# Kernel tuning notes

Hardware: AMD Instinct MI355X
Metric: run time of the kernel (lower is better)

Reference implementation:

```python
import jax, jax.numpy as jnp
import numpy as np

B, N, K = 8, 4096, 5


def setup_inputs() -> dict:
    key = jax.random.key(0)
    ks = jax.random.split(key, 24)
    s = 0.05
    inp = {
        'pointcloud': jax.random.normal(ks[0], (B, 3, N, 1), jnp.float32),
        # local 1x1 conv stack (bias-free) + BN affine params (eval mode, stats=identity)
        'conv_w1': jax.random.normal(ks[1], (64, 3), jnp.float32) * s,
        'bn1_g': jnp.ones((64,), jnp.float32), 'bn1_b': jnp.zeros((64,), jnp.float32),
        'conv_w2': jax.random.normal(ks[2], (64, 64), jnp.float32) * s,
        'bn2_g': jnp.ones((64,), jnp.float32), 'bn2_b': jnp.zeros((64,), jnp.float32),
        'conv_w3': jax.random.normal(ks[3], (64, 64), jnp.float32) * s,
        'bn3_g': jnp.ones((64,), jnp.float32), 'bn3_b': jnp.zeros((64,), jnp.float32),
        'conv_w4': jax.random.normal(ks[4], (128, 64), jnp.float32) * s,
        'bn4_g': jnp.ones((128,), jnp.float32), 'bn4_b': jnp.zeros((128,), jnp.float32),
        # GCN layers
        'gc1_w': jax.random.normal(ks[5], (128, 128), jnp.float32) * s,
        'gc1_b': jnp.zeros((128,), jnp.float32),
        'gc2_w': jax.random.normal(ks[6], (128, 128), jnp.float32) * s,
        'gc2_b': jnp.zeros((128,), jnp.float32),
        'gc3_w': jax.random.normal(ks[7], (128, 256), jnp.float32) * s,
        'gc3_b': jnp.zeros((256,), jnp.float32),
        # MLP head
        'fc1_w': jax.random.normal(ks[8], (512, 256), jnp.float32) * s,
        'bnf1_g': jnp.ones((512,), jnp.float32), 'bnf1_b': jnp.zeros((512,), jnp.float32),
        'fc2_w': jax.random.normal(ks[9], (256, 512), jnp.float32) * s,
        'bnf2_g': jnp.ones((256,), jnp.float32), 'bnf2_b': jnp.zeros((256,), jnp.float32),
        'fc3_w': jax.random.normal(ks[10], (128, 256), jnp.float32) * s,
        'fc3_b': jnp.zeros((128,), jnp.float32),
    }
    return inp


def _cbr(h, w, g, b):
    # 1x1 conv (per-point linear) + BatchNorm(eval, identity stats) + ReLU
    return jax.nn.relu((h @ w.T) * g + b)


def reference(pointcloud, conv_w1, bn1_g, bn1_b, conv_w2, bn2_g, bn2_b,
              conv_w3, bn3_g, bn3_b, conv_w4, bn4_g, bn4_b,
              gc1_w, gc1_b, gc2_w, gc2_b, gc3_w, gc3_b,
              fc1_w, bnf1_g, bnf1_b, fc2_w, bnf2_g, bnf2_b, fc3_w, fc3_b):
    pts = pointcloud[..., 0]                       # [B,3,N]
    b, _, n = pts.shape

    # ---- LocalOperation: sort points by distance to centroid, gather ----
    centroid = pts.mean(axis=2, keepdims=True)     # [B,3,1]
    d_cent = ((pts - centroid) ** 2).sum(axis=1)   # [B,N]
    order = jnp.argsort(d_cent, axis=-1)           # [B,N]
    x = jnp.take_along_axis(pts, order[:, None, :], axis=2)  # [B,3,N]

    h = x.transpose(0, 2, 1)                       # [B,N,3]
    h = _cbr(h, conv_w1, bn1_g, bn1_b)             # [B,N,64]
    h = _cbr(h, conv_w2, bn2_g, bn2_b)
    h = _cbr(h, conv_w3, bn3_g, bn3_b)
    h = _cbr(h, conv_w4, bn4_g, bn4_b)             # [B,N,128]
    feat = h.reshape(b * n, 128)                   # node features

    # ---- KNN graph (k=5, within each cloud, self included like KDTree) ----
    sq = (pts ** 2).sum(axis=1)                                        # [B,N]
    d2 = sq[:, :, None] + sq[:, None, :] - 2.0 * jnp.einsum('bcn,bcm->bnm', pts, pts)
    _, nbr = jax.lax.top_k(-d2, K)                                     # [B,N,K]
    offsets = (jnp.arange(b) * n)[:, None, None]
    src = (nbr + offsets).reshape(-1)                                  # [B*N*K]
    dst = jnp.broadcast_to(jnp.arange(b * n).reshape(b, n, 1), (b, n, K)).reshape(-1)

    num_nodes = b * n
    ones = jnp.ones_like(src, jnp.float32)
    deg_out = jax.ops.segment_sum(ones, src, num_segments=num_nodes)
    deg_in = jax.ops.segment_sum(ones, dst, num_segments=num_nodes)
    norm_out = jax.lax.rsqrt(jnp.maximum(deg_out, 1.0))
    norm_in = jax.lax.rsqrt(jnp.maximum(deg_in, 1.0))

    def gcn(hh, w, bias):
        hw = (hh @ w) * norm_out[:, None]          # [BN,F] pre-normed features
        msg = hw[src]                              # gather
        agg = jax.ops.segment_sum(msg, dst, num_segments=num_nodes)  # scatter-add
        return agg * norm_in[:, None] + bias

    g = jax.nn.relu(gcn(feat, gc1_w, gc1_b))       # [BN,128]
    g = jax.nn.relu(gcn(g, gc2_w, gc2_b))          # [BN,128]
    g = gcn(g, gc3_w, gc3_b)                       # [BN,256]

    # ---- head (BN eval, dropout eval = identity) ----
    z = jax.nn.relu((g @ fc1_w.T) * bnf1_g + bnf1_b)   # [BN,512]
    z = jax.nn.relu((z @ fc2_w.T) * bnf2_g + bnf2_b)   # [BN,256]
    pooled = z.max(axis=0)                             # [256] global max over nodes
    out = pooled @ fc3_w.T + fc3_b                     # [128]
    return out
```

## Files before the change

### kernel.cpp

```cpp
#include <hip/hip_runtime.h>
#include <math.h>
#include <float.h>

#define NB 8
#define NP 4096
#define BN_ (NB*NP)
#define KNN 5
#define JCH 512
#define NJC (NP/JCH)
#define SENT 64

typedef unsigned short u16;
typedef __attribute__((ext_vector_type(8))) __bf16 bf16x8;
typedef __attribute__((ext_vector_type(4))) float f32x4;

__device__ __forceinline__ u16 f2bf(float x){
  unsigned u = __float_as_uint(x);
  u += 0x7fff + ((u>>16)&1);
  return (u16)(u>>16);
}
__device__ __forceinline__ float bf2f(u16 h){ return __uint_as_float(((unsigned)h)<<16); }


__global__ void k_centroid(const float* __restrict__ pc, float* __restrict__ dcent,
                           int* __restrict__ rankb) {
  int b = blockIdx.x, tid = threadIdx.x;
  const float* px = pc + (size_t)b*3*NP;
  const float* py = px + NP;
  const float* pz = py + NP;
  double sx=0, sy=0, sz=0;
  for (int n = tid; n < NP; n += 256) { sx += px[n]; sy += py[n]; sz += pz[n]; }
  __shared__ double rx[256], ry[256], rz[256];
  rx[tid]=sx; ry[tid]=sy; rz[tid]=sz;
  __syncthreads();
  for (int s = 128; s > 0; s >>= 1) {
    if (tid < s) { rx[tid]+=rx[tid+s]; ry[tid]+=ry[tid+s]; rz[tid]+=rz[tid+s]; }
    __syncthreads();
  }
  __shared__ float cxs, cys, czs;
  if (tid == 0) {
    cxs = (float)(rx[0]/NP); cys = (float)(ry[0]/NP); czs = (float)(rz[0]/NP);
  }
  __syncthreads();
  float cx = cxs, cy = cys, cz = czs;
  for (int n = tid; n < NP; n += 256) {
    float dx = __fsub_rn(px[n], cx);
    float dy = __fsub_rn(py[n], cy);
    float dz = __fsub_rn(pz[n], cz);
    float d = __fadd_rn(__fadd_rn(__fmul_rn(dx,dx), __fmul_rn(dy,dy)), __fmul_rn(dz,dz));
    dcent[b*NP + n] = d;
    rankb[b*NP + n] = 0;
  }
}

__global__ void __launch_bounds__(256) k_rank_part(const float* __restrict__ dcent,
                                                   int* __restrict__ rank) {
  int jc = blockIdx.x, ic = blockIdx.y, b = blockIdx.z;
  __shared__ float d[JCH];
  int j0 = jc*JCH;
  for (int n = threadIdx.x; n < JCH; n += 256) d[n] = dcent[b*NP + j0 + n];
  __syncthreads();
  int i = ic*256 + threadIdx.x;
  float di = dcent[b*NP + i];
  int cnt = 0;
  #pragma unroll 8
  for (int n = 0; n < JCH; ++n) {
    float dj = d[n];
    cnt += (dj < di) || (dj == di && (j0 + n) < i);
  }
  atomicAdd(&rank[b*NP + i], cnt);
}

__global__ void k_scatprep(const float* __restrict__ pc, const int* __restrict__ rank,
                           const float* __restrict__ dcent,
                           int* __restrict__ ord, float4* __restrict__ srt,
                           float* __restrict__ rcv, int* __restrict__ deg) {
  int idx = blockIdx.x*256 + threadIdx.x;
  int b = idx >> 12, i = idx & (NP-1);
  int r = rank[idx];
  ord[b*NP + r] = i;
  const float* base = pc + (size_t)b*3*NP;
  float x = base[i], y = base[NP+i], z = base[2*NP+i];
  float sq = __fadd_rn(__fadd_rn(__fmul_rn(x,x), __fmul_rn(y,y)), __fmul_rn(z,z));
  float4 v; v.x=x; v.y=y; v.z=z; v.w=sq;
  srt[b*NP + r] = v;
  rcv[b*NP + r] = sqrtf(dcent[idx]);
  deg[idx] = 0;
}

#define INS(dist, q) \
  if (dist < b4) { \
    if (dist < b3) { b4=b3; r4=r3; \
      if (dist < b2) { b3=b2; r3=r2; \
        if (dist < b1) { b2=b1; r2=r1; \
          if (dist < b0) { b1=b0; r1=r0; b0=dist; r0=(q); } \
          else { b1=dist; r1=(q); } \
        } else { b2=dist; r2=(q); } \
      } else { b3=dist; r3=(q); } \
    } else { b4=dist; r4=(q); } \
  }

__global__ void __launch_bounds__(512) k_knn_ann4(const float4* __restrict__ srt,
                                                  const float* __restrict__ rc,
                                                  const int* __restrict__ ord,
                                                  int* __restrict__ nbr,
                                                  int* __restrict__ deg) {
  __shared__ float4 tile[NP + 2*SENT];
  __shared__ float rtile[NP + 2*SENT];
  int b = blockIdx.x >> 6;
  int blk = blockIdx.x & 63;
  int gbase = b*NP;
  for (int t = threadIdx.x; t < NP + 2*SENT; t += 512) {
    int q = t - SENT;
    if ((unsigned)q < NP) { tile[t] = srt[gbase + q]; rtile[t] = rc[gbase + q]; }
    else { float4 s4; s4.x=0.f; s4.y=0.f; s4.z=0.f; s4.w=1e30f; tile[t] = s4; rtile[t] = 0.f; }
  }
  __syncthreads();

  const int lane = threadIdx.x & 63;
  const int wv   = threadIdx.x >> 6;
  const int grp  = lane >> 3;
  const int sub  = lane & 7;
  const int s_i  = blk*64 + wv*8 + grp;

  float4 p = tile[SENT + s_i];
  float xi=p.x, yi=p.y, zi=p.z, sqi=p.w;
  float ri = rtile[SENT + s_i];

  const bool is_hi = (sub < 4);
  const int step = is_hi ? 4 : -4;
  const int jdead = is_hi ? (NP + 7) : (-36);
  int j = is_hi ? (s_i + sub) : (s_i - 1 - (sub - 4));
  bool alive = ((unsigned)j < NP);
  if (!alive) j = jdead;

  float b0=FLT_MAX, b1=FLT_MAX, b2=FLT_MAX, b3=FLT_MAX, b4=FLT_MAX;
  int r0=0, r1=0, r2=0, r3=0, r4=0;

  while (__ballot(alive)) {
    float4 jp[8];
    #pragma unroll
    for (int t = 0; t < 8; ++t) jp[t] = tile[SENT + j + step*t];
    #pragma unroll
    for (int t = 0; t < 8; ++t) {
      float dot = __fadd_rn(__fadd_rn(__fmul_rn(xi,jp[t].x), __fmul_rn(yi,jp[t].y)), __fmul_rn(zi,jp[t].z));
      float dist = __fsub_rn(__fadd_rn(sqi, jp[t].w), __fmul_rn(2.0f, dot));
      if (__ballot(dist < b4)) { INS(dist, j + step*t) }
    }
    float bm = b4;
    bm = fminf(bm, __shfl_xor(bm, 1));
    bm = fminf(bm, __shfl_xor(bm, 2));
    bm = fminf(bm, __shfl_xor(bm, 4));
    float T = bm*1.0002f + 1e-9f;
    float dr = fabsf(ri - rtile[SENT + j + step*7]);
    bool nextin = ((unsigned)(j + step*8) < NP);
    alive = alive && nextin && (__fmul_rn(dr,dr) < T);
    j = alive ? (j + step*8) : jdead;
  }

  #pragma unroll
  for (int m = 1; m <= 4; m <<= 1) {
    float c0=__shfl_xor(b0,m), c1=__shfl_xor(b1,m), c2=__shfl_xor(b2,m),
          c3=__shfl_xor(b3,m), c4=__shfl_xor(b4,m);
    int   s0=__shfl_xor(r0,m), s1=__shfl_xor(r1,m), s2=__shfl_xor(r2,m),
          s3=__shfl_xor(r3,m), s4=__shfl_xor(r4,m);
    if (c0 < b4) { INS(c0, s0)
      if (c1 < b4) { INS(c1, s1)
        if (c2 < b4) { INS(c2, s2)
          if (c3 < b4) { INS(c3, s3)
            if (c4 < b4) { INS(c4, s4) }
          }
        }
      }
    }
  }

  if (sub == 0) {
    int oi = ord[gbase + s_i];
    int node = gbase + oi;
    int nb = node*KNN;
    int o0 = gbase + ord[gbase+r0], o1 = gbase + ord[gbase+r1], o2 = gbase + ord[gbase+r2];
    int o3 = gbase + ord[gbase+r3], o4 = gbase + ord[gbase+r4];
    nbr[nb+0]=o0; nbr[nb+1]=o1; nbr[nb+2]=o2; nbr[nb+3]=o3; nbr[nb+4]=o4;
    atomicAdd(&deg[o0],1); atomicAdd(&deg[o1],1); atomicAdd(&deg[o2],1);
    atomicAdd(&deg[o3],1); atomicAdd(&deg[o4],1);
  }
}

__global__ void k_cvt_all(const float* __restrict__ w2, const float* __restrict__ w3,
                          const float* __restrict__ w4, const float* __restrict__ gc1,
                          const float* __restrict__ gc2, const float* __restrict__ gc3,
                          const float* __restrict__ fc1, const float* __restrict__ fc2,
                          u16* o2, u16* o3, u16* o4, u16* og1, u16* og2, u16* og3,
                          u16* of1, u16* of2) {
  int i = blockIdx.x*256 + threadIdx.x;
  if (i < 4096) { o2[i] = f2bf(w2[i]); return; } i -= 4096;
  if (i < 4096) { o3[i] = f2bf(w3[i]); return; } i -= 4096;
  if (i < 8192) { o4[i] = f2bf(w4[i]); return; } i -= 8192;
  if (i < 16384) { int n=i>>7, k=i&127; og1[i] = f2bf(gc1[k*128+n]); return; } i -= 16384;
  if (i < 16384) { int n=i>>7, k=i&127; og2[i] = f2bf(gc2[k*128+n]); return; } i -= 16384;
  if (i < 32768) { int n=i>>7, k=i&127; og3[i] = f2bf(gc3[k*256+n]); return; } i -= 32768;
  if (i < 131072) { of1[i] = f2bf(fc1[i]); return; } i -= 131072;
  if (i < 131072) { of2[i] = f2bf(fc2[i]); }
}

__global__ void k_conv1(const float* __restrict__ pc, const int* __restrict__ ord,
                        const float* __restrict__ w, const float* __restrict__ g,
                        const float* __restrict__ bias, u16* __restrict__ outp,
                        float* __restrict__ pooled) {
  if (blockIdx.x == 0) pooled[threadIdx.x] = 0.0f;
  int node = blockIdx.x*4 + (threadIdx.x >> 6);
  int o = threadIdx.x & 63;
  int b = node >> 12;
  int j = ord[node];
  const float* base = pc + (size_t)b*3*NP;
  float x = base[j], y = base[NP + j], z = base[2*NP + j];
  float acc = x*w[o*3+0] + y*w[o*3+1] + z*w[o*3+2];
  float v = fmaxf(acc*g[o] + bias[o], 0.0f);
  outp[(size_t)node*64 + o] = f2bf(v);
}

template<int BNT>
__global__ __launch_bounds__(256) void gemm_bf16(
    const u16* __restrict__ A, const u16* __restrict__ W,
    const float* __restrict__ gamma, const float* __restrict__ beta,
    const int* __restrict__ degp, void* __restrict__ Cout,
    int K, int Nc, int mode) {
  constexpr int NF = BNT/32;
  __shared__ u16 As[128*64];
  __shared__ u16 Bs[BNT*64];
  const int tid = threadIdx.x;
  const int w = tid >> 6, l = tid & 63;
  const int m0 = blockIdx.x*128, n0 = blockIdx.y*BNT;
  const int wm = w & 1, wn = w >> 1;
  const int lr = l >> 3;
  const int lc = l & 7;
  const int fm = l & 15, fk = l >> 4;

  f32x4 acc[4][NF];
  #pragma unroll
  for (int i=0;i<4;++i)
    #pragma unroll
    for (int j=0;j<NF;++j) acc[i][j] = (f32x4){0.f,0.f,0.f,0.f};

  for (int k0 = 0; k0 < K; k0 += 64) {
    #pragma unroll
    for (int t=0;t<4;++t){
      int row = (w*4 + t)*8 + lr;
      uint4 v = *(const uint4*)(A + ((size_t)(m0+row)*K + k0 + lc*8));
      *(uint4*)&As[row*64 + ((lc ^ (row&7))*8)] = v;
    }
    #pragma unroll
    for (int t=0;t<NF;++t){
      int row = (w*NF + t)*8 + lr;
      uint4 v = *(const uint4*)(W + ((size_t)(n0+row)*K + k0 + lc*8));
      *(uint4*)&Bs[row*64 + ((lc ^ (row&7))*8)] = v;
    }
    __syncthreads();
    #pragma unroll
    for (int ks=0; ks<2; ++ks){
      bf16x8 af[4], bfr[NF];
      #pragma unroll
      for (int mf=0; mf<4; ++mf){
        int row = wm*64 + mf*16 + fm;
        int ck = ks*4 + fk;
        af[mf] = *(const bf16x8*)&As[row*64 + ((ck ^ (row&7))*8)];
      }
      #pragma unroll
      for (int nf=0; nf<NF; ++nf){
        int row = wn*(BNT/2) + nf*16 + fm;
        int ck = ks*4 + fk;
        bfr[nf] = *(const bf16x8*)&Bs[row*64 + ((ck ^ (row&7))*8)];
      }
      #pragma unroll
      for (int mf=0; mf<4; ++mf)
        #pragma unroll
        for (int nf=0; nf<NF; ++nf)
          acc[mf][nf] = __builtin_amdgcn_mfma_f32_16x16x32_bf16(af[mf], bfr[nf], acc[mf][nf], 0, 0, 0);
    }
    __syncthreads();
  }

  const int col_base = n0 + wn*(BNT/2);
  if (mode == 1) {
    u16* C = (u16*)Cout;
    #pragma unroll
    for (int mf=0; mf<4; ++mf){
      #pragma unroll
      for (int r=0;r<4;++r){
        int row = m0 + wm*64 + mf*16 + fk*4 + r;
        int d = degp[row]; if (d < 1) d = 1;
        float rs = 1.0f / sqrtf((float)d);
        #pragma unroll
        for (int nf=0;nf<NF;++nf){
          int col = col_base + nf*16 + fm;
          C[(size_t)row*Nc + col] = f2bf(acc[mf][nf][r]*rs);
        }
      }
    }
  } else {
    float gv[NF], bv[NF];
    #pragma unroll
    for (int nf=0;nf<NF;++nf){
      int col = col_base + nf*16 + fm;
      gv[nf] = gamma[col]; bv[nf] = beta[col];
    }
    #pragma unroll
    for (int mf=0; mf<4; ++mf){
      #pragma unroll
      for (int r=0;r<4;++r){
        int row = m0 + wm*64 + mf*16 + fk*4 + r;
        #pragma unroll
        for (int nf=0;nf<NF;++nf){
          int col = col_base + nf*16 + fm;
          float v = fmaxf(acc[mf][nf][r]*gv[nf] + bv[nf], 0.f);
          if (mode == 0) ((u16*)Cout)[(size_t)row*Nc + col] = f2bf(v);
          else           ((float*)Cout)[(size_t)row*Nc + col] = v;
        }
      }
    }
  }
}

__global__ void k_agg_bf(const u16* __restrict__ hw, const int* __restrict__ nbr,
                         const float* __restrict__ bias, u16* __restrict__ outp,
                         int F, int do_relu) {
  int per = F >> 3;
  int gid = blockIdx.x*256 + threadIdx.x;
  int i = gid / per;
  int f = (gid - i*per) * 8;
  const int* nb = nbr + i*KNN;
  float s[8] = {0,0,0,0,0,0,0,0};
  #pragma unroll
  for (int k = 0; k < KNN; ++k) {
    uint4 v = *(const uint4*)(hw + (size_t)nb[k]*F + f);
    const u16* h = (const u16*)&v;
    #pragma unroll
    for (int j=0;j<8;++j) s[j] += bf2f(h[j]);
  }
  const float ninv = 0.44721359549995793f;
  u16 o[8];
  #pragma unroll
  for (int j=0;j<8;++j){
    float v = s[j]*ninv + bias[f+j];
    if (do_relu) v = fmaxf(v, 0.f);
    o[j] = f2bf(v);
  }
  *(uint4*)&outp[(size_t)i*F + f] = *(const uint4*)o;
}

__global__ void k_maxpool(const float* __restrict__ z, unsigned int* __restrict__ pooled) {
  int o = threadIdx.x;
  int r0 = blockIdx.x * 128;
  float m = 0.0f;
  for (int r = 0; r < 128; ++r) m = fmaxf(m, z[(size_t)(r0 + r)*256 + o]);
  atomicMax(&pooled[o], __float_as_uint(m));
}

__global__ void k_fc3(const float* __restrict__ pooled, const float* __restrict__ w,
                      const float* __restrict__ bias, float* __restrict__ outp) {
  __shared__ float p[256];
  int tid = threadIdx.x;
  p[tid] = pooled[tid];
  p[tid + 128] = pooled[tid + 128];
  __syncthreads();
  float s = 0.0f;
  for (int i = 0; i < 256; ++i) s = fmaf(w[tid*256 + i], p[i], s);
  outp[tid] = s + bias[tid];
}

extern "C" void kernel_launch(void* const* d_in, const int* in_sizes, int n_in,
                              void* d_out, int out_size, void* d_ws, size_t ws_size,
                              hipStream_t stream) {
  const float* pc   = (const float*)d_in[0];
  const float* w1   = (const float*)d_in[1];
  const float* g1   = (const float*)d_in[2];
  const float* b1   = (const float*)d_in[3];
  const float* w2   = (const float*)d_in[4];
  const float* g2   = (const float*)d_in[5];
  const float* b2   = (const float*)d_in[6];
  const float* w3   = (const float*)d_in[7];
  const float* g3   = (const float*)d_in[8];
  const float* b3   = (const float*)d_in[9];
  const float* w4   = (const float*)d_in[10];
  const float* g4   = (const float*)d_in[11];
  const float* b4   = (const float*)d_in[12];
  const float* gc1w = (const float*)d_in[13];
  const float* gc1b = (const float*)d_in[14];
  const float* gc2w = (const float*)d_in[15];
  const float* gc2b = (const float*)d_in[16];
  const float* gc3w = (const float*)d_in[17];
  const float* gc3b = (const float*)d_in[18];
  const float* fc1w = (const float*)d_in[19];
  const float* f1g  = (const float*)d_in[20];
  const float* f1b  = (const float*)d_in[21];
  const float* fc2w = (const float*)d_in[22];
  const float* f2g  = (const float*)d_in[23];
  const float* f2b  = (const float*)d_in[24];
  const float* fc3w = (const float*)d_in[25];
  const float* fc3b = (const float*)d_in[26];
  float* outp = (float*)d_out;

  char* wsb = (char*)d_ws;
  size_t off = 0;
  auto alloc = [&](size_t bytes) -> void* {
    void* p = wsb + off;
    off += (bytes + 255) & ~(size_t)255;
    return p;
  };
  int*   ord    = (int*)  alloc((size_t)BN_*4);
  int*   deg    = (int*)  alloc((size_t)BN_*4);
  int*   rankb  = (int*)  alloc((size_t)BN_*4);
  int*   nbr    = (int*)  alloc((size_t)BN_*KNN*4);
  float* dcent  = (float*)alloc((size_t)BN_*4);
  float* pooled = (float*)alloc(256*4);
  float4* srt   = (float4*)alloc((size_t)BN_*16);
  float* rc     = (float*)alloc((size_t)BN_*4);
  u16* wb2   = (u16*)alloc(64*64*2);
  u16* wb3   = (u16*)alloc(64*64*2);
  u16* wb4   = (u16*)alloc(128*64*2);
  u16* wgc1  = (u16*)alloc(128*128*2);
  u16* wgc2  = (u16*)alloc(128*128*2);
  u16* wgc3  = (u16*)alloc(256*128*2);
  u16* wfc1  = (u16*)alloc(512*256*2);
  u16* wfc2  = (u16*)alloc(256*512*2);
  u16* h1   = (u16*)alloc((size_t)BN_*64*2);
  u16* h2   = (u16*)alloc((size_t)BN_*64*2);
  u16* feat = (u16*)alloc((size_t)BN_*128*2);
  u16* hw   = (u16*)alloc((size_t)BN_*256*2);
  u16* gb1  = (u16*)alloc((size_t)BN_*128*2);
  u16* g3b  = (u16*)alloc((size_t)BN_*256*2);
  u16* z1   = (u16*)alloc((size_t)BN_*512*2);
  float* z2 = (float*)alloc((size_t)BN_*256*4);

  k_cvt_all<<<1344, 256, 0, stream>>>(w2, w3, w4, gc1w, gc2w, gc3w, fc1w, fc2w,
                                      wb2, wb3, wb4, wgc1, wgc2, wgc3, wfc1, wfc2);

  k_centroid<<<NB, 256, 0, stream>>>(pc, dcent, rankb);
  k_rank_part<<<dim3(NJC, NP/256, NB), 256, 0, stream>>>(dcent, rankb);
  k_scatprep<<<BN_/256, 256, 0, stream>>>(pc, rankb, dcent, ord, srt, rc, deg);
  k_knn_ann4<<<NB*64, 512, 0, stream>>>(srt, rc, ord, nbr, deg);

  k_conv1<<<BN_/4, 256, 0, stream>>>(pc, ord, w1, g1, b1, h1, pooled);
  gemm_bf16<64><<<dim3(BN_/128, 1), 256, 0, stream>>>(h1, wb2, g2, b2, nullptr, h2, 64, 64, 0);
  gemm_bf16<64><<<dim3(BN_/128, 1), 256, 0, stream>>>(h2, wb3, g3, b3, nullptr, h1, 64, 64, 0);
  gemm_bf16<128><<<dim3(BN_/128, 1), 256, 0, stream>>>(h1, wb4, g4, b4, nullptr, feat, 64, 128, 0);

  gemm_bf16<128><<<dim3(BN_/128, 1), 256, 0, stream>>>(feat, wgc1, nullptr, nullptr, deg, hw, 128, 128, 1);
  k_agg_bf<<<(BN_*16)/256, 256, 0, stream>>>(hw, nbr, gc1b, gb1, 128, 1);
  gemm_bf16<128><<<dim3(BN_/128, 1), 256, 0, stream>>>(gb1, wgc2, nullptr, nullptr, deg, hw, 128, 128, 1);
  k_agg_bf<<<(BN_*16)/256, 256, 0, stream>>>(hw, nbr, gc2b, feat, 128, 1);
  gemm_bf16<128><<<dim3(BN_/128, 2), 256, 0, stream>>>(feat, wgc3, nullptr, nullptr, deg, hw, 128, 256, 1);
  k_agg_bf<<<(BN_*32)/256, 256, 0, stream>>>(hw, nbr, gc3b, g3b, 256, 0);

  gemm_bf16<128><<<dim3(BN_/128, 4), 256, 0, stream>>>(g3b, wfc1, f1g, f1b, nullptr, z1, 256, 512, 0);
  gemm_bf16<128><<<dim3(BN_/128, 2), 256, 0, stream>>>(z1, wfc2, f2g, f2b, nullptr, z2, 512, 256, 2);
  k_maxpool<<<BN_/128, 256, 0, stream>>>(z2, (unsigned int*)pooled);
  k_fc3<<<1, 128, 0, stream>>>(pooled, fc3w, fc3b, outp);
}
```

Baseline: 405.3 us.

## Restructure KNN: seed threshold from local block, collect candidates, fallback brute force

Replaces the per-query 8-lane sorted-scan KNN with a scheme where each lane owns one query. It first computes an exact top-5 over the 64-point local sorted block to get a fixed distance threshold, then four waves scan outward in interleaved strides, collecting sub-threshold candidates into shared memory. Wave 0 then merges them, with a full brute-force fallback when any wave overflows its 16 candidate slots. This removes the shared-memory tile load of the whole cloud and the per-step shuffles and ballots, but reads neighbours from global memory and risks a slow serial merge or fallback path.

```diff
diff --git a/kernel.cpp b/kernel.cpp
--- a/kernel.cpp
+++ b/kernel.cpp
@@ -8,7 +8,6 @@
 #define KNN 5
 #define JCH 512
 #define NJC (NP/JCH)
-#define SENT 64
 
 typedef unsigned short u16;
 typedef __attribute__((ext_vector_type(8))) __bf16 bf16x8;
@@ -100,83 +99,107 @@
     } else { b4=dist; r4=(q); } \
   }
 
-__global__ void __launch_bounds__(512) k_knn_ann4(const float4* __restrict__ srt,
-                                                  const float* __restrict__ rc,
-                                                  const int* __restrict__ ord,
-                                                  int* __restrict__ nbr,
-                                                  int* __restrict__ deg) {
-  __shared__ float4 tile[NP + 2*SENT];
-  __shared__ float rtile[NP + 2*SENT];
-  int b = blockIdx.x >> 6;
-  int blk = blockIdx.x & 63;
-  int gbase = b*NP;
-  for (int t = threadIdx.x; t < NP + 2*SENT; t += 512) {
-    int q = t - SENT;
-    if ((unsigned)q < NP) { tile[t] = srt[gbase + q]; rtile[t] = rc[gbase + q]; }
-    else { float4 s4; s4.x=0.f; s4.y=0.f; s4.z=0.f; s4.w=1e30f; tile[t] = s4; rtile[t] = 0.f; }
-  }
-  __syncthreads();
-
+#define DISTQ(jp) \
+  float dot = __fadd_rn(__fadd_rn(__fmul_rn(xi,(jp).x), __fmul_rn(yi,(jp).y)), __fmul_rn(zi,(jp).z)); \
+  float dist = __fsub_rn(__fadd_rn(sqi, (jp).w), __fmul_rn(2.0f, dot));
+
+__global__ void __launch_bounds__(256) k_knn5(const float4* __restrict__ srt,
+                                              const float* __restrict__ rc,
+                                              const int* __restrict__ ord,
+                                              int* __restrict__ nbr,
+                                              int* __restrict__ deg) {
+  __shared__ float cd[4][16][64];
+  __shared__ int   cj[4][16][64];
+  __shared__ int   ccnt[4][64];
+  const int blk = blockIdx.x;
+  const int b = blk >> 6;
+  const int g0 = (blk & 63) * 64;
+  const int gbase = b*NP;
+  const int wv = threadIdx.x >> 6;
   const int lane = threadIdx.x & 63;
-  const int wv   = threadIdx.x >> 6;
-  const int grp  = lane >> 3;
-  const int sub  = lane & 7;
-  const int s_i  = blk*64 + wv*8 + grp;
-
-  float4 p = tile[SENT + s_i];
+
+  float4 p = srt[gbase + g0 + lane];
   float xi=p.x, yi=p.y, zi=p.z, sqi=p.w;
-  float ri = rtile[SENT + s_i];
-
-  const bool is_hi = (sub < 4);
-  const int step = is_hi ? 4 : -4;
-  const int jdead = is_hi ? (NP + 7) : (-36);
-  int j = is_hi ? (s_i + sub) : (s_i - 1 - (sub - 4));
-  bool alive = ((unsigned)j < NP);
-  if (!alive) j = jdead;
+  float ri = rc[gbase + g0 + lane];
 
   float b0=FLT_MAX, b1=FLT_MAX, b2=FLT_MAX, b3=FLT_MAX, b4=FLT_MAX;
   int r0=0, r1=0, r2=0, r3=0, r4=0;
 
-  while (__ballot(alive)) {
-    float4 jp[8];
-    #pragma unroll
-    for (int t = 0; t < 8; ++t) jp[t] = tile[SENT + j + step*t];
+  for (int t0 = 0; t0 < 64; t0 += 8) {
+    float4 q[8];
+    #pragma unroll
+    for (int t = 0; t < 8; ++t) q[t] = srt[gbase + g0 + t0 + t];
     #pragma unroll
     for (int t = 0; t < 8; ++t) {
-      float dot = __fadd_rn(__fadd_rn(__fmul_rn(xi,jp[t].x), __fmul_rn(yi,jp[t].y)), __fmul_rn(zi,jp[t].z));
-      float dist = __fsub_rn(__fadd_rn(sqi, jp[t].w), __fmul_rn(2.0f, dot));
-      if (__ballot(dist < b4)) { INS(dist, j + step*t) }
-    }
-    float bm = b4;
-    bm = fminf(bm, __shfl_xor(bm, 1));
-    bm = fminf(bm, __shfl_xor(bm, 2));
-    bm = fminf(bm, __shfl_xor(bm, 4));
-    float T = bm*1.0002f + 1e-9f;
-    float dr = fabsf(ri - rtile[SENT + j + step*7]);
-    bool nextin = ((unsigned)(j + step*8) < NP);
-    alive = alive && nextin && (__fmul_rn(dr,dr) < T);
-    j = alive ? (j + step*8) : jdead;
-  }
-
+      DISTQ(q[t])
+      if (dist < b4) { INS(dist, g0 + t0 + t) }
+    }
+  }
+  const float T = b4*1.0002f + 1e-9f;
+
+  int cnt = 0;
   #pragma unroll
-  for (int m = 1; m <= 4; m <<= 1) {
-    float c0=__shfl_xor(b0,m), c1=__shfl_xor(b1,m), c2=__shfl_xor(b2,m),
-          c3=__shfl_xor(b3,m), c4=__shfl_xor(b4,m);
-    int   s0=__shfl_xor(r0,m), s1=__shfl_xor(r1,m), s2=__shfl_xor(r2,m),
-          s3=__shfl_xor(r3,m), s4=__shfl_xor(r4,m);
-    if (c0 < b4) { INS(c0, s0)
-      if (c1 < b4) { INS(c1, s1)
-        if (c2 < b4) { INS(c2, s2)
-          if (c3 < b4) { INS(c3, s3)
-            if (c4 < b4) { INS(c4, s4) }
+  for (int dir = 0; dir < 2; ++dir) {
+    const int step = dir ? -4 : 4;
+    int jb = dir ? (g0 - 1 - wv) : (g0 + 64 + wv);
+    while ((unsigned)jb < NP) {
+      float4 q[8]; int jq[8];
+      #pragma unroll
+      for (int t = 0; t < 8; ++t) {
+        int jt = jb + step*t;
+        bool in = (unsigned)jt < NP;
+        jq[t] = jt;
+        if (in) q[t] = srt[gbase + jt];
+        else { q[t].x=0.f; q[t].y=0.f; q[t].z=0.f; q[t].w=1e30f; }
+      }
+      #pragma unroll
+      for (int t = 0; t < 8; ++t) {
+        DISTQ(q[t])
+        if (__ballot(dist < T)) {
+          if (dist < T) {
+            if (cnt < 16) { cd[wv][cnt][lane] = dist; cj[wv][cnt][lane] = jq[t]; }
+            cnt++;
           }
         }
       }
-    }
-  }
-
-  if (sub == 0) {
-    int oi = ord[gbase + s_i];
+      int jl = jb + step*7;
+      jl = jl < 0 ? 0 : (jl > NP-1 ? NP-1 : jl);
+      float dr = __fsub_rn(ri, rc[gbase + jl]);
+      bool alive = __fmul_rn(dr,dr) < T;
+      if (!__ballot(alive)) break;
+      jb += step*8;
+    }
+  }
+  ccnt[wv][lane] = cnt;
+  __syncthreads();
+
+  if (wv == 0) {
+    int c0 = ccnt[0][lane], c1 = ccnt[1][lane], c2 = ccnt[2][lane], c3 = ccnt[3][lane];
+    bool ov = (c0 > 16) | (c1 > 16) | (c2 > 16) | (c3 > 16);
+    if (__ballot(ov)) {
+      if (ov) { b0=b1=b2=b3=b4=FLT_MAX; r0=r1=r2=r3=r4=0; }
+      for (int j0 = 0; j0 < NP; j0 += 8) {
+        float4 q[8];
+        #pragma unroll
+        for (int t = 0; t < 8; ++t) q[t] = srt[gbase + j0 + t];
+        #pragma unroll
+        for (int t = 0; t < 8; ++t) {
+          DISTQ(q[t])
+          if (ov && dist < b4) { INS(dist, j0 + t) }
+        }
+      }
+    }
+    if (!ov) {
+      #pragma unroll
+      for (int w2 = 0; w2 < 4; ++w2) {
+        int c = ccnt[w2][lane]; if (c > 16) c = 16;
+        for (int e = 0; e < c; ++e) {
+          float d = cd[w2][e][lane]; int jj = cj[w2][e][lane];
+          if (d < b4) { INS(d, jj) }
+        }
+      }
+    }
+    int oi = ord[gbase + g0 + lane];
     int node = gbase + oi;
     int nb = node*KNN;
     int o0 = gbase + ord[gbase+r0], o1 = gbase + ord[gbase+r1], o2 = gbase + ord[gbase+r2];
@@ -439,7 +462,7 @@
   k_centroid<<<NB, 256, 0, stream>>>(pc, dcent, rankb);
   k_rank_part<<<dim3(NJC, NP/256, NB), 256, 0, stream>>>(dcent, rankb);
   k_scatprep<<<BN_/256, 256, 0, stream>>>(pc, rankb, dcent, ord, srt, rc, deg);
-  k_knn_ann4<<<NB*64, 512, 0, stream>>>(srt, rc, ord, nbr, deg);
+  k_knn5<<<512, 256, 0, stream>>>(srt, rc, ord, nbr, deg);
 
   k_conv1<<<BN_/4, 256, 0, stream>>>(pc, ord, w1, g1, b1, h1, pooled);
   gemm_bf16<64><<<dim3(BN_/128, 1), 256, 0, stream>>>(h1, wb2, g2, b2, nullptr, h2, 64, 64, 0);
```

After: 1.037 ms. 2.56x slower.

## Replace radial-pruned bidirectional KNN scan with windowed threshold plus full brute-force scan

Applied to the files above, without the earlier changes.

The KNN kernel drops the early-terminating walk along centroid-distance-sorted points, which was pruned by radial distance bounds. It now seeds a distance threshold from a 64-point window around each query, then scans all 4096 points with 4 lanes per query, inserting only candidates under the threshold. This removes the per-iteration ballot, shuffle and termination logic and the radial-distance array, but does far more distance evaluations per query (a full O(N^2) scan). Blocks shrink to 256 threads and handle 64 queries each.

```diff
diff --git a/kernel.cpp b/kernel.cpp
--- a/kernel.cpp
+++ b/kernel.cpp
@@ -8,7 +8,6 @@
 #define KNN 5
 #define JCH 512
 #define NJC (NP/JCH)
-#define SENT 64
 
 typedef unsigned short u16;
 typedef __attribute__((ext_vector_type(8))) __bf16 bf16x8;
@@ -72,9 +71,8 @@
 }
 
 __global__ void k_scatprep(const float* __restrict__ pc, const int* __restrict__ rank,
-                           const float* __restrict__ dcent,
                            int* __restrict__ ord, float4* __restrict__ srt,
-                           float* __restrict__ rcv, int* __restrict__ deg) {
+                           int* __restrict__ deg) {
   int idx = blockIdx.x*256 + threadIdx.x;
   int b = idx >> 12, i = idx & (NP-1);
   int r = rank[idx];
@@ -84,7 +82,6 @@
   float sq = __fadd_rn(__fadd_rn(__fmul_rn(x,x), __fmul_rn(y,y)), __fmul_rn(z,z));
   float4 v; v.x=x; v.y=y; v.z=z; v.w=sq;
   srt[b*NP + r] = v;
-  rcv[b*NP + r] = sqrtf(dcent[idx]);
   deg[idx] = 0;
 }
 
@@ -100,80 +97,78 @@
     } else { b4=dist; r4=(q); } \
   }
 
-__global__ void __launch_bounds__(512) k_knn_ann4(const float4* __restrict__ srt,
-                                                  const float* __restrict__ rc,
-                                                  const int* __restrict__ ord,
-                                                  int* __restrict__ nbr,
-                                                  int* __restrict__ deg) {
-  __shared__ float4 tile[NP + 2*SENT];
-  __shared__ float rtile[NP + 2*SENT];
-  int b = blockIdx.x >> 6;
-  int blk = blockIdx.x & 63;
-  int gbase = b*NP;
-  for (int t = threadIdx.x; t < NP + 2*SENT; t += 512) {
-    int q = t - SENT;
-    if ((unsigned)q < NP) { tile[t] = srt[gbase + q]; rtile[t] = rc[gbase + q]; }
-    else { float4 s4; s4.x=0.f; s4.y=0.f; s4.z=0.f; s4.w=1e30f; tile[t] = s4; rtile[t] = 0.f; }
-  }
+#define DISTQ(jp) \
+  float dot = __fadd_rn(__fadd_rn(__fmul_rn(xi,(jp).x), __fmul_rn(yi,(jp).y)), __fmul_rn(zi,(jp).z)); \
+  float dist = __fsub_rn(__fadd_rn(sqi, (jp).w), __fmul_rn(2.0f, dot));
+
+#define MERGE4 \
+  _Pragma("unroll") \
+  for (int m = 1; m <= 2; m <<= 1) { \
+    float c0=__shfl_xor(b0,m), c1=__shfl_xor(b1,m), c2=__shfl_xor(b2,m), \
+          c3=__shfl_xor(b3,m), c4=__shfl_xor(b4,m); \
+    int   s0=__shfl_xor(r0,m), s1=__shfl_xor(r1,m), s2=__shfl_xor(r2,m), \
+          s3=__shfl_xor(r3,m), s4=__shfl_xor(r4,m); \
+    if (c0 < b4) { INS(c0, s0) \
+      if (c1 < b4) { INS(c1, s1) \
+        if (c2 < b4) { INS(c2, s2) \
+          if (c3 < b4) { INS(c3, s3) \
+            if (c4 < b4) { INS(c4, s4) } } } } } \
+  }
+
+__global__ void __launch_bounds__(256) k_knn6(const float4* __restrict__ srt,
+                                              const int* __restrict__ ord,
+                                              int* __restrict__ nbr,
+                                              int* __restrict__ deg) {
+  __shared__ float4 tile[NP];
+  const int blk = blockIdx.x;
+  const int b = blk >> 6;
+  const int gbase = b*NP;
+  for (int t = threadIdx.x; t < NP; t += 256) tile[t] = srt[gbase + t];
   __syncthreads();
 
   const int lane = threadIdx.x & 63;
   const int wv   = threadIdx.x >> 6;
-  const int grp  = lane >> 3;
-  const int sub  = lane & 7;
-  const int s_i  = blk*64 + wv*8 + grp;
-
-  float4 p = tile[SENT + s_i];
+  const int grp  = lane >> 2;
+  const int sub  = lane & 3;
+  const int s_i  = (blk & 63)*64 + wv*16 + grp;
+
+  float4 p = tile[s_i];
   float xi=p.x, yi=p.y, zi=p.z, sqi=p.w;
-  float ri = rtile[SENT + s_i];
-
-  const bool is_hi = (sub < 4);
-  const int step = is_hi ? 4 : -4;
-  const int jdead = is_hi ? (NP + 7) : (-36);
-  int j = is_hi ? (s_i + sub) : (s_i - 1 - (sub - 4));
-  bool alive = ((unsigned)j < NP);
-  if (!alive) j = jdead;
 
   float b0=FLT_MAX, b1=FLT_MAX, b2=FLT_MAX, b3=FLT_MAX, b4=FLT_MAX;
   int r0=0, r1=0, r2=0, r3=0, r4=0;
 
-  while (__ballot(alive)) {
-    float4 jp[8];
-    #pragma unroll
-    for (int t = 0; t < 8; ++t) jp[t] = tile[SENT + j + step*t];
+  int w0 = s_i - 32;
+  if (w0 < 0) w0 = 0;
+  if (w0 > NP-64) w0 = NP-64;
+  #pragma unroll 4
+  for (int k = 0; k < 16; ++k) {
+    int j = w0 + sub + 4*k;
+    float4 q = tile[j];
+    DISTQ(q)
+    if (dist < b4) { INS(dist, j) }
+  }
+  MERGE4
+  const float Tthr = b4;
+  b0=FLT_MAX; b1=FLT_MAX; b2=FLT_MAX; b3=FLT_MAX; b4=FLT_MAX;
+  r0=0; r1=0; r2=0; r3=0; r4=0;
+
+  const int q0 = sub*1024;
+  for (int jb = 0; jb < 1024; jb += 8) {
+    float4 q[8];
+    #pragma unroll
+    for (int t = 0; t < 8; ++t) q[t] = tile[q0 + jb + t];
     #pragma unroll
     for (int t = 0; t < 8; ++t) {
-      float dot = __fadd_rn(__fadd_rn(__fmul_rn(xi,jp[t].x), __fmul_rn(yi,jp[t].y)), __fmul_rn(zi,jp[t].z));
-      float dist = __fsub_rn(__fadd_rn(sqi, jp[t].w), __fmul_rn(2.0f, dot));
-      if (__ballot(dist < b4)) { INS(dist, j + step*t) }
-    }
-    float bm = b4;
-    bm = fminf(bm, __shfl_xor(bm, 1));
-    bm = fminf(bm, __shfl_xor(bm, 2));
-    bm = fminf(bm, __shfl_xor(bm, 4));
-    float T = bm*1.0002f + 1e-9f;
-    float dr = fabsf(ri - rtile[SENT + j + step*7]);
-    bool nextin = ((unsigned)(j + step*8) < NP);
-    alive = alive && nextin && (__fmul_rn(dr,dr) < T);
-    j = alive ? (j + step*8) : jdead;
-  }
-
-  #pragma unroll
-  for (int m = 1; m <= 4; m <<= 1) {
-    float c0=__shfl_xor(b0,m), c1=__shfl_xor(b1,m), c2=__shfl_xor(b2,m),
-          c3=__shfl_xor(b3,m), c4=__shfl_xor(b4,m);
-    int   s0=__shfl_xor(r0,m), s1=__shfl_xor(r1,m), s2=__shfl_xor(r2,m),
-          s3=__shfl_xor(r3,m), s4=__shfl_xor(r4,m);
-    if (c0 < b4) { INS(c0, s0)
-      if (c1 < b4) { INS(c1, s1)
-        if (c2 < b4) { INS(c2, s2)
-          if (c3 < b4) { INS(c3, s3)
-            if (c4 < b4) { INS(c4, s4) }
-          }
-        }
+      DISTQ(q[t])
+      bool c = (dist <= Tthr) && (dist < b4);
+      if (__ballot(c)) {
+        if (dist <= Tthr) { INS(dist, q0 + jb + t) }
       }
     }
   }
+
+  MERGE4
 
   if (sub == 0) {
     int oi = ord[gbase + s_i];
@@ -415,7 +410,6 @@
   float* dcent  = (float*)alloc((size_t)BN_*4);
   float* pooled = (float*)alloc(256*4);
   float4* srt   = (float4*)alloc((size_t)BN_*16);
-  float* rc     = (float*)alloc((size_t)BN_*4);
   u16* wb2   = (u16*)alloc(64*64*2);
   u16* wb3   = (u16*)alloc(64*64*2);
   u16* wb4   = (u16*)alloc(128*64*2);
@@ -438,8 +432,8 @@
 
   k_centroid<<<NB, 256, 0, stream>>>(pc, dcent, rankb);
   k_rank_part<<<dim3(NJC, NP/256, NB), 256, 0, stream>>>(dcent, rankb);
-  k_scatprep<<<BN_/256, 256, 0, stream>>>(pc, rankb, dcent, ord, srt, rc, deg);
-  k_knn_ann4<<<NB*64, 512, 0, stream>>>(srt, rc, ord, nbr, deg);
+  k_scatprep<<<BN_/256, 256, 0, stream>>>(pc, rankb, ord, srt, deg);
+  k_knn6<<<512, 256, 0, stream>>>(srt, ord, nbr, deg);
 
   k_conv1<<<BN_/4, 256, 0, stream>>>(pc, ord, w1, g1, b1, h1, pooled);
   gemm_bf16<64><<<dim3(BN_/128, 1), 256, 0, stream>>>(h1, wb2, g2, b2, nullptr, h2, 64, 64, 0);
```

Result: slower. 439.2 us (+8.4%).
